# Kernel optimization log

Measured on AMD Instinct MI355X. Metric: run time of the kernel, lower is better.

## Reference

```python
import jax, jax.numpy as jnp
import numpy as np

N_NODES = 50000
N_EDGES = 800000
NEG_SLOPE = 0.2  # PyG GATConv default leaky_relu slope


def gat_conv(x, edge_index, W, a_src, a_dst, b, concat):
    """PyG-style GATConv with self-loops already included in edge_index.
    x: [N, F_in], W: [F_in, H*C], a_src/a_dst: [H, C], b: [H*C] or [C]."""
    N = x.shape[0]
    H, C = a_src.shape
    xw = (x @ W).reshape(N, H, C)                       # [N, H, C]
    src, dst = edge_index[0], edge_index[1]
    alpha_s = jnp.einsum('nhc,hc->nh', xw, a_src)       # [N, H]
    alpha_d = jnp.einsum('nhc,hc->nh', xw, a_dst)
    e = jax.nn.leaky_relu(alpha_s[src] + alpha_d[dst], NEG_SLOPE)  # [E, H]
    # segment softmax over incoming edges of each dst node
    emax = jax.ops.segment_max(e, dst, num_segments=N)  # [N, H]
    p = jnp.exp(e - emax[dst])
    denom = jax.ops.segment_sum(p, dst, num_segments=N)
    alpha = p / (denom[dst] + 1e-16)                    # [E, H]
    msg = xw[src] * alpha[..., None]                    # [E, H, C]
    out = jax.ops.segment_sum(msg, dst, num_segments=N) # [N, H, C]
    out = out.reshape(N, H * C) if concat else out.mean(axis=1)
    return out + b


def setup_inputs() -> dict:
    key = jax.random.key(0)
    ks = jax.random.split(key, 12)
    s = 0.1
    x = jax.random.normal(ks[0], (N_NODES, 128), dtype=jnp.float32)
    edge_index = jax.random.randint(ks[1], (2, N_EDGES), 0, N_NODES, dtype=jnp.int64)
    return {
        'x': x,
        'edge_index': edge_index,
        'W1': jax.random.normal(ks[2], (128, 64), jnp.float32) * s,
        'a1_src': jax.random.normal(ks[3], (8, 8), jnp.float32) * s,
        'a1_dst': jax.random.normal(ks[4], (8, 8), jnp.float32) * s,
        'b1': jnp.zeros((64,), jnp.float32),
        'W2': jax.random.normal(ks[5], (64, 64), jnp.float32) * s,
        'a2_src': jax.random.normal(ks[6], (8, 8), jnp.float32) * s,
        'a2_dst': jax.random.normal(ks[7], (8, 8), jnp.float32) * s,
        'b2': jnp.zeros((64,), jnp.float32),
        'W3': jax.random.normal(ks[8], (64, 242), jnp.float32) * s,
        'a3_src': jax.random.normal(ks[9], (1, 242), jnp.float32) * s,
        'a3_dst': jax.random.normal(ks[10], (1, 242), jnp.float32) * s,
        'b3': jnp.zeros((242,), jnp.float32),
    }


def reference(x, edge_index, W1, a1_src, a1_dst, b1, W2, a2_src, a2_dst, b2,
              W3, a3_src, a3_dst, b3):
    N = x.shape[0]
    # PyG GATConv adds self-loops by default
    loops = jnp.arange(N, dtype=edge_index.dtype)
    ei = jnp.concatenate([edge_index, jnp.stack([loops, loops])], axis=1)
    h = jax.nn.relu(gat_conv(x, ei, W1, a1_src, a1_dst, b1, concat=True))
    # dropout is identity in eval mode
    h = jax.nn.relu(gat_conv(h, ei, W2, a2_src, a2_dst, b2, concat=True))
    h = jax.nn.relu(gat_conv(h, ei, W3, a3_src, a3_dst, b3, concat=False))
    h = h.reshape(N, -1, 2)                             # [N, num_classes, 2]
    return jax.nn.softmax(h, axis=-1)
```

## Files before the change

kernel.cpp:

```cpp
#include <hip/hip_runtime.h>
#include <hip/hip_bf16.h>
#include <hip/hip_fp16.h>


#define CH 4096
#define CAP 8192

__device__ __forceinline__ float lrelu(float s) { return (s >= 0.f) ? s : 0.2f * s; }


__global__ void detect_kernel(const int* __restrict__ ei, int* __restrict__ flag) {
    int t = threadIdx.x;
    int v = ei[2 * t + 1];
    unsigned long long b = __ballot(v == 0);
    if (t == 0) *flag = (b == ~0ULL) ? 1 : 0;
}

__device__ __forceinline__ int edge_at(const void* ei, int is64, long long idx) {
    return is64 ? (int)((const long long*)ei)[idx] : ((const int*)ei)[idx];
}


__global__ void zero_btot_kernel(int* __restrict__ btot) {
    btot[threadIdx.x] = 0;
}

__global__ __launch_bounds__(256)
void histA_kernel(const void* __restrict__ ei, const int* __restrict__ flag,
                  int* __restrict__ blkhist, int* __restrict__ btot, int E, int N) {
    __shared__ int h[256];
    int t = threadIdx.x;
    h[t] = 0;
    __syncthreads();
    int is64 = *flag;
    long long base = (long long)blockIdx.x * CH;
    long long tot = (long long)E + N;
#pragma unroll
    for (int i = 0; i < CH / 256; ++i) {
        long long idx = base + t + i * 256;
        if (idx < tot) {
            int dst = (idx < E) ? edge_at(ei, is64, (long long)E + idx) : (int)(idx - E);
            atomicAdd(&h[(dst >> 8) & 255], 1);
        }
    }
    __syncthreads();
    int nb = (N + 255) >> 8;
    if (t < nb) {
        blkhist[t * 256 + blockIdx.x] = h[t];
        atomicAdd(&btot[t], h[t]);
    }
}

__global__ __launch_bounds__(256)
void bucket_scan_kernel(const int* __restrict__ btot, int* __restrict__ bbase,
                        int nb, int total) {
    __shared__ int s[256];
    int t = threadIdx.x;
    int v = (t < nb) ? btot[t] : 0;
    s[t] = v;
    __syncthreads();
#pragma unroll
    for (int off = 1; off < 256; off <<= 1) {
        int u = (t >= off) ? s[t - off] : 0;
        __syncthreads();
        s[t] += u;
        __syncthreads();
    }
    if (t < nb) bbase[t] = s[t] - v;
    if (t == 0) bbase[nb] = total;
}

__global__ __launch_bounds__(256)
void blk_scan_kernel(const int* __restrict__ blkhist, const int* __restrict__ bbase,
                     int* __restrict__ blkoff, int nblk) {
    __shared__ int s[256];
    int t = threadIdx.x;
    int b = blockIdx.x;
    int v = (t < nblk) ? blkhist[b * 256 + t] : 0;
    s[t] = v;
    __syncthreads();
#pragma unroll
    for (int off = 1; off < 256; off <<= 1) {
        int u = (t >= off) ? s[t - off] : 0;
        __syncthreads();
        s[t] += u;
        __syncthreads();
    }
    if (t < nblk) blkoff[b * 256 + t] = bbase[b] + s[t] - v;
}

__global__ __launch_bounds__(256)
void partC_kernel(const void* __restrict__ ei, const int* __restrict__ flag,
                  const int* __restrict__ blkoff, int2* __restrict__ part,
                  int E, int N) {
    __shared__ int h[256];
    __shared__ int lst[256];
    __shared__ int cur[256];
    __shared__ int grb[256];
    __shared__ int ssrc[CH];
    __shared__ int sdst[CH];
    int t = threadIdx.x;
    h[t] = 0;
    __syncthreads();
    int is64 = *flag;
    long long base = (long long)blockIdx.x * CH;
    long long tot = (long long)E + N;
    int msrc[CH / 256], mdst[CH / 256], mb[CH / 256];
#pragma unroll
    for (int i = 0; i < CH / 256; ++i) {
        long long idx = base + t + i * 256;
        if (idx < tot) {
            int s, d;
            if (idx < E) {
                s = edge_at(ei, is64, idx);
                d = edge_at(ei, is64, (long long)E + idx);
            } else {
                s = (int)(idx - E);
                d = s;
            }
            msrc[i] = s;
            mdst[i] = d;
            mb[i] = (d >> 8) & 255;
            atomicAdd(&h[mb[i]], 1);
        } else {
            mb[i] = -1;
        }
    }
    __syncthreads();
    int v = h[t];
    lst[t] = v;
    __syncthreads();
#pragma unroll
    for (int off = 1; off < 256; off <<= 1) {
        int u = (t >= off) ? lst[t - off] : 0;
        __syncthreads();
        lst[t] += u;
        __syncthreads();
    }
    int ex = lst[t] - v;
    lst[t] = ex;
    cur[t] = ex;
    int nb = (N + 255) >> 8;
    grb[t] = (t < nb) ? blkoff[t * 256 + blockIdx.x] : 0;
    __syncthreads();
#pragma unroll
    for (int i = 0; i < CH / 256; ++i) {
        if (mb[i] >= 0) {
            int slot = atomicAdd(&cur[mb[i]], 1);
            ssrc[slot] = msrc[i];
            sdst[slot] = mdst[i];
        }
    }
    __syncthreads();
    int items = (int)((tot - base < CH) ? (tot - base) : CH);
    for (int r = t; r < items; r += 256) {
        int d = sdst[r];
        int b = (d >> 8) & 255;
        part[grb[b] + (r - lst[b])] = make_int2(ssrc[r], d);
    }
}

__global__ __launch_bounds__(256)
void csrD_kernel(const int2* __restrict__ part, const int* __restrict__ bbase,
                 int* __restrict__ row_ptr, int* __restrict__ adj, int N) {
    __shared__ int cnt[256];
    __shared__ int lst[256];
    __shared__ int cur[256];
    __shared__ int ssrc[CAP];
    int t = threadIdx.x;
    int b = blockIdx.x;
    int lo = bbase[b], hi = bbase[b + 1];
    int n0 = b << 8;
    cnt[t] = 0;
    __syncthreads();
    for (int r = lo + t; r < hi; r += 256) atomicAdd(&cnt[part[r].y & 255], 1);
    __syncthreads();
    int v = cnt[t];
    lst[t] = v;
    __syncthreads();
#pragma unroll
    for (int off = 1; off < 256; off <<= 1) {
        int u = (t >= off) ? lst[t - off] : 0;
        __syncthreads();
        lst[t] += u;
        __syncthreads();
    }
    int ex = lst[t] - v;
    lst[t] = ex;
    cur[t] = ex;
    __syncthreads();
    if (n0 + t < N) row_ptr[n0 + t] = lo + ex;
    if (b == gridDim.x - 1 && t == 0) row_ptr[N] = hi;
    int items = hi - lo;
    if (items <= CAP) {
        for (int r = lo + t; r < hi; r += 256) {
            int2 p = part[r];
            int slot = atomicAdd(&cur[p.y & 255], 1);
            ssrc[slot] = p.x;
        }
        __syncthreads();
        for (int r = t; r < items; r += 256) adj[lo + r] = ssrc[r];
    } else {
        for (int r = lo + t; r < hi; r += 256) {
            int2 p = part[r];
            int slot = atomicAdd(&cur[p.y & 255], 1);
            adj[lo + slot] = p.x;
        }
    }
}


__global__ void w3a_kernel(const float* __restrict__ W3,
                           const float* __restrict__ a3s,
                           const float* __restrict__ a3d,
                           float* __restrict__ w_as, float* __restrict__ w_ad) {
    int t = threadIdx.x;
    if (t >= 128) return;
    int k = t & 63;
    const float* a = (t < 64) ? a3s : a3d;
    float s = 0.f;
    for (int c = 0; c < 242; ++c) s = fmaf(W3[k * 242 + c], a[c], s);
    if (t < 64) w_as[k] = s; else w_ad[k] = s;
}

__global__ __launch_bounds__(256)
void w3pad_kernel(const float* __restrict__ W3, float* __restrict__ W3p) {
    int t = blockIdx.x * blockDim.x + threadIdx.x;
    if (t >= 64 * 244) return;
    int k = t / 244, c = t - k * 244;
    W3p[t] = (c < 242) ? W3[k * 242 + c] : 0.f;
}


template <int K>
__global__ __launch_bounds__(256)
void gemm_alpha_v5(const float* __restrict__ X, const float* __restrict__ W,
                   const float* __restrict__ a_src, const float* __restrict__ a_dst,
                   __half* __restrict__ XWh, float* __restrict__ As, float* __restrict__ Ad,
                   int N) {
    constexpr int S = K + 4;
    constexpr int F4R = K / 4;
    __shared__ float xs[32][S];
    int t = threadIdx.x;
    int block0 = blockIdx.x * 32;

    for (int i = t; i < 32 * F4R; i += 256) {
        int row = i / F4R, c4 = i - row * F4R;
        int node = block0 + row;
        float4 v = (node < N) ? *(const float4*)(X + (size_t)node * K + c4 * 4)
                              : make_float4(0.f, 0.f, 0.f, 0.f);
        *(float4*)(&xs[row][c4 * 4]) = v;
    }
    __syncthreads();

    int wave = t >> 6, lane = t & 63;
    int jj = lane >> 4, cc = lane & 15;
    int r0 = wave * 8 + jj * 2;
    int base = block0 + r0;

    float4 o0 = make_float4(0.f, 0.f, 0.f, 0.f);
    float4 o1 = make_float4(0.f, 0.f, 0.f, 0.f);

    const float* wp = W + cc * 4;
#pragma unroll 2
    for (int k = 0; k < K; k += 4) {
        float4 w0 = *(const float4*)(wp + (size_t)(k + 0) * 64);
        float4 w1 = *(const float4*)(wp + (size_t)(k + 1) * 64);
        float4 w2 = *(const float4*)(wp + (size_t)(k + 2) * 64);
        float4 w3 = *(const float4*)(wp + (size_t)(k + 3) * 64);
        float4 m0 = *(const float4*)(&xs[r0][k]);
        float4 m1 = *(const float4*)(&xs[r0 + 1][k]);

        o0.x = fmaf(m0.x, w0.x, o0.x);
        o0.y = fmaf(m0.x, w0.y, o0.y);
        o0.z = fmaf(m0.x, w0.z, o0.z);
        o0.w = fmaf(m0.x, w0.w, o0.w);
        o0.x = fmaf(m0.y, w1.x, o0.x);
        o0.y = fmaf(m0.y, w1.y, o0.y);
        o0.z = fmaf(m0.y, w1.z, o0.z);
        o0.w = fmaf(m0.y, w1.w, o0.w);
        o0.x = fmaf(m0.z, w2.x, o0.x);
        o0.y = fmaf(m0.z, w2.y, o0.y);
        o0.z = fmaf(m0.z, w2.z, o0.z);
        o0.w = fmaf(m0.z, w2.w, o0.w);
        o0.x = fmaf(m0.w, w3.x, o0.x);
        o0.y = fmaf(m0.w, w3.y, o0.y);
        o0.z = fmaf(m0.w, w3.z, o0.z);
        o0.w = fmaf(m0.w, w3.w, o0.w);

        o1.x = fmaf(m1.x, w0.x, o1.x);
        o1.y = fmaf(m1.x, w0.y, o1.y);
        o1.z = fmaf(m1.x, w0.z, o1.z);
        o1.w = fmaf(m1.x, w0.w, o1.w);
        o1.x = fmaf(m1.y, w1.x, o1.x);
        o1.y = fmaf(m1.y, w1.y, o1.y);
        o1.z = fmaf(m1.y, w1.z, o1.z);
        o1.w = fmaf(m1.y, w1.w, o1.w);
        o1.x = fmaf(m1.z, w2.x, o1.x);
        o1.y = fmaf(m1.z, w2.y, o1.y);
        o1.z = fmaf(m1.z, w2.z, o1.z);
        o1.w = fmaf(m1.z, w2.w, o1.w);
        o1.x = fmaf(m1.w, w3.x, o1.x);
        o1.y = fmaf(m1.w, w3.y, o1.y);
        o1.z = fmaf(m1.w, w3.z, o1.z);
        o1.w = fmaf(m1.w, w3.w, o1.w);
    }

    float4 av = *(const float4*)(a_src + cc * 4);
    float4 dv = *(const float4*)(a_dst + cc * 4);

    if (base < N) {
        union { __half2 h[2]; uint2 u; } pk;
        pk.h[0] = __floats2half2_rn(o0.x, o0.y);
        pk.h[1] = __floats2half2_rn(o0.z, o0.w);
        *(uint2*)(XWh + (size_t)base * 64 + cc * 4) = pk.u;
        float s = o0.x * av.x + o0.y * av.y + o0.z * av.z + o0.w * av.w;
        float d = o0.x * dv.x + o0.y * dv.y + o0.z * dv.z + o0.w * dv.w;
        s += __shfl_xor(s, 1);
        d += __shfl_xor(d, 1);
        if ((cc & 1) == 0) {
            As[base * 8 + (cc >> 1)] = s;
            Ad[base * 8 + (cc >> 1)] = d;
        }
    }
    if (base + 1 < N) {
        union { __half2 h[2]; uint2 u; } pk;
        pk.h[0] = __floats2half2_rn(o1.x, o1.y);
        pk.h[1] = __floats2half2_rn(o1.z, o1.w);
        *(uint2*)(XWh + (size_t)(base + 1) * 64 + cc * 4) = pk.u;
        float s = o1.x * av.x + o1.y * av.y + o1.z * av.z + o1.w * av.w;
        float d = o1.x * dv.x + o1.y * dv.y + o1.z * dv.z + o1.w * dv.w;
        s += __shfl_xor(s, 1);
        d += __shfl_xor(d, 1);
        if ((cc & 1) == 0) {
            As[(base + 1) * 8 + (cc >> 1)] = s;
            Ad[(base + 1) * 8 + (cc >> 1)] = d;
        }
    }
}


template <bool WITH_A3, bool HALF_OUT>
__global__ __launch_bounds__(256)
void agg_h8c8_v3(const __half* __restrict__ XW, const float* __restrict__ As,
                 const float* __restrict__ Ad, const int* __restrict__ row_ptr,
                 const int* __restrict__ adj, const float* __restrict__ bias,
                 void* __restrict__ OUTv,
                 const float* __restrict__ w_as, const float* __restrict__ w_ad,
                 float* __restrict__ As3, float* __restrict__ Ad3, int N) {
    int wave = threadIdx.x >> 6, lane = threadIdx.x & 63;
    int node = blockIdx.x * 4 + wave;
    if (node >= N) return;
    int beg = row_ptr[node], end = row_ptr[node + 1];
    int eP = lane >> 3, hP = lane & 7;
    int hA = lane >> 3;
    float adp = Ad[node * 8 + hP];
    float bv = bias[lane];

    float den_part = 0.f;
    float acc0 = 0.f, acc1 = 0.f;
    int idx = beg;
    for (; idx + 8 <= end; idx += 8) {
        int se = adj[idx + eP];
        float ec = As[(size_t)se * 8 + hP];
        float p = __expf(lrelu(ec + adp));
        den_part += p;
        int s0 = adj[idx + 0], s1 = adj[idx + 1], s2 = adj[idx + 2], s3 = adj[idx + 3];
        int s4 = adj[idx + 4], s5 = adj[idx + 5], s6 = adj[idx + 6], s7 = adj[idx + 7];
        float x0 = __half2float(XW[(size_t)s0 * 64 + lane]);
        float x1 = __half2float(XW[(size_t)s1 * 64 + lane]);
        float x2 = __half2float(XW[(size_t)s2 * 64 + lane]);
        float x3 = __half2float(XW[(size_t)s3 * 64 + lane]);
        float x4 = __half2float(XW[(size_t)s4 * 64 + lane]);
        float x5 = __half2float(XW[(size_t)s5 * 64 + lane]);
        float x6 = __half2float(XW[(size_t)s6 * 64 + lane]);
        float x7 = __half2float(XW[(size_t)s7 * 64 + lane]);
        float p0 = __shfl(p, 0 * 8 + hA);
        float p1 = __shfl(p, 1 * 8 + hA);
        float p2 = __shfl(p, 2 * 8 + hA);
        float p3 = __shfl(p, 3 * 8 + hA);
        float p4 = __shfl(p, 4 * 8 + hA);
        float p5 = __shfl(p, 5 * 8 + hA);
        float p6 = __shfl(p, 6 * 8 + hA);
        float p7 = __shfl(p, 7 * 8 + hA);
        acc0 = fmaf(p0, x0, acc0);
        acc1 = fmaf(p1, x1, acc1);
        acc0 = fmaf(p2, x2, acc0);
        acc1 = fmaf(p3, x3, acc1);
        acc0 = fmaf(p4, x4, acc0);
        acc1 = fmaf(p5, x5, acc1);
        acc0 = fmaf(p6, x6, acc0);
        acc1 = fmaf(p7, x7, acc1);
    }
    int rem = end - idx;
    if (rem > 0) {
        int se = adj[idx + (eP < rem ? eP : rem - 1)];
        float ec = As[(size_t)se * 8 + hP];
        float p = (eP < rem) ? __expf(lrelu(ec + adp)) : 0.f;
        den_part += p;
#pragma unroll
        for (int k = 0; k < 8; ++k) {
            if (k < rem) {
                int sk = adj[idx + k];
                float xk = __half2float(XW[(size_t)sk * 64 + lane]);
                float pk = __shfl(p, k * 8 + hA);
                acc0 = fmaf(pk, xk, acc0);
            }
        }
    }
    float acc = acc0 + acc1;
    den_part += __shfl_xor(den_part, 8);
    den_part += __shfl_xor(den_part, 16);
    den_part += __shfl_xor(den_part, 32);
    float den = __shfl(den_part, hA);

    float v = fmaxf(acc / (den + 1e-16f) + bv, 0.f);
    if (HALF_OUT) ((__half*)OUTv)[(size_t)node * 64 + lane] = __float2half_rn(v);
    else          ((float*)OUTv)[(size_t)node * 64 + lane] = v;

    if (WITH_A3) {
        float s3v = v * w_as[lane];
        float d3v = v * w_ad[lane];
#pragma unroll
        for (int m = 1; m <= 32; m <<= 1) {
            s3v += __shfl_xor(s3v, m);
            d3v += __shfl_xor(d3v, m);
        }
        if (lane == 0) {
            As3[node] = s3v;
            Ad3[node] = d3v;
        }
    }
}


__global__ __launch_bounds__(256)
void agg3msg_v3(const __half* __restrict__ H2, const float* __restrict__ As3,
                const float* __restrict__ Ad3, const int* __restrict__ row_ptr,
                const int* __restrict__ adj, float* __restrict__ MSG, int N) {
    int wave = threadIdx.x >> 6, lane = threadIdx.x & 63;
    int node = blockIdx.x * 4 + wave;
    if (node >= N) return;
    int beg = row_ptr[node], end = row_ptr[node + 1];
    float ad = Ad3[node];
    int eP = lane & 7;
    int gbase = lane & 56;

    float den_part = 0.f;
    float acc0 = 0.f, acc1 = 0.f;
    int idx = beg;
    for (; idx + 8 <= end; idx += 8) {
        int se = adj[idx + eP];
        float p = __expf(lrelu(As3[se] + ad));
        den_part += p;
        int s0 = adj[idx + 0], s1 = adj[idx + 1], s2 = adj[idx + 2], s3 = adj[idx + 3];
        int s4 = adj[idx + 4], s5 = adj[idx + 5], s6 = adj[idx + 6], s7 = adj[idx + 7];
        float x0 = __half2float(H2[(size_t)s0 * 64 + lane]);
        float x1 = __half2float(H2[(size_t)s1 * 64 + lane]);
        float x2 = __half2float(H2[(size_t)s2 * 64 + lane]);
        float x3 = __half2float(H2[(size_t)s3 * 64 + lane]);
        float x4 = __half2float(H2[(size_t)s4 * 64 + lane]);
        float x5 = __half2float(H2[(size_t)s5 * 64 + lane]);
        float x6 = __half2float(H2[(size_t)s6 * 64 + lane]);
        float x7 = __half2float(H2[(size_t)s7 * 64 + lane]);
        float p0 = __shfl(p, gbase + 0);
        float p1 = __shfl(p, gbase + 1);
        float p2 = __shfl(p, gbase + 2);
        float p3 = __shfl(p, gbase + 3);
        float p4 = __shfl(p, gbase + 4);
        float p5 = __shfl(p, gbase + 5);
        float p6 = __shfl(p, gbase + 6);
        float p7 = __shfl(p, gbase + 7);
        acc0 = fmaf(p0, x0, acc0);
        acc1 = fmaf(p1, x1, acc1);
        acc0 = fmaf(p2, x2, acc0);
        acc1 = fmaf(p3, x3, acc1);
        acc0 = fmaf(p4, x4, acc0);
        acc1 = fmaf(p5, x5, acc1);
        acc0 = fmaf(p6, x6, acc0);
        acc1 = fmaf(p7, x7, acc1);
    }
    int rem = end - idx;
    if (rem > 0) {
        int se = adj[idx + (eP < rem ? eP : rem - 1)];
        float p = (eP < rem) ? __expf(lrelu(As3[se] + ad)) : 0.f;
        den_part += p;
#pragma unroll
        for (int k = 0; k < 8; ++k) {
            if (k < rem) {
                int sk = adj[idx + k];
                float xk = __half2float(H2[(size_t)sk * 64 + lane]);
                float pk = __shfl(p, gbase + k);
                acc0 = fmaf(pk, xk, acc0);
            }
        }
    }
    float acc = acc0 + acc1;
    den_part += __shfl_xor(den_part, 1);
    den_part += __shfl_xor(den_part, 2);
    den_part += __shfl_xor(den_part, 4);
    MSG[(size_t)node * 64 + lane] = acc / (den_part + 1e-16f);
}


__global__ __launch_bounds__(256)
void gemm3_kernel(const float* __restrict__ MSG, const float* __restrict__ W3p,
                  const float* __restrict__ bias, float* __restrict__ OUT, int N) {
    __shared__ float msh[4][8][64];
    int wave = threadIdx.x >> 6, lane = threadIdx.x & 63;
    int base = blockIdx.x * 32 + wave * 8;

#pragma unroll
    for (int j = 0; j < 8; ++j) {
        int node = base + j;
        msh[wave][j][lane] = (node < N) ? MSG[(size_t)node * 64 + lane] : 0.f;
    }

    int c0 = lane * 4;
    if (c0 < 242) {
        float o[8][4];
#pragma unroll
        for (int j = 0; j < 8; ++j)
#pragma unroll
            for (int q = 0; q < 4; ++q) o[j][q] = 0.f;

#pragma unroll 4
        for (int k = 0; k < 64; k += 4) {
            float4 w0 = *(const float4*)(W3p + (size_t)(k + 0) * 244 + c0);
            float4 w1 = *(const float4*)(W3p + (size_t)(k + 1) * 244 + c0);
            float4 w2 = *(const float4*)(W3p + (size_t)(k + 2) * 244 + c0);
            float4 w3 = *(const float4*)(W3p + (size_t)(k + 3) * 244 + c0);
#pragma unroll
            for (int j = 0; j < 8; ++j) {
                float4 m = *(const float4*)(&msh[wave][j][k]);
                o[j][0] = fmaf(m.x, w0.x, o[j][0]);
                o[j][1] = fmaf(m.x, w0.y, o[j][1]);
                o[j][2] = fmaf(m.x, w0.z, o[j][2]);
                o[j][3] = fmaf(m.x, w0.w, o[j][3]);
                o[j][0] = fmaf(m.y, w1.x, o[j][0]);
                o[j][1] = fmaf(m.y, w1.y, o[j][1]);
                o[j][2] = fmaf(m.y, w1.z, o[j][2]);
                o[j][3] = fmaf(m.y, w1.w, o[j][3]);
                o[j][0] = fmaf(m.z, w2.x, o[j][0]);
                o[j][1] = fmaf(m.z, w2.y, o[j][1]);
                o[j][2] = fmaf(m.z, w2.z, o[j][2]);
                o[j][3] = fmaf(m.z, w2.w, o[j][3]);
                o[j][0] = fmaf(m.w, w3.x, o[j][0]);
                o[j][1] = fmaf(m.w, w3.y, o[j][1]);
                o[j][2] = fmaf(m.w, w3.z, o[j][2]);
                o[j][3] = fmaf(m.w, w3.w, o[j][3]);
            }
        }

        float b0 = bias[c0], b1v = bias[c0 + 1];
        float b2v = (c0 + 2 < 242) ? bias[c0 + 2] : 0.f;
        float b3v = (c0 + 3 < 242) ? bias[c0 + 3] : 0.f;
#pragma unroll
        for (int j = 0; j < 8; ++j) {
            int node = base + j;
            if (node >= N) break;
            size_t out_base = (size_t)node * 242 + c0;
            float v0 = fmaxf(o[j][0] + b0, 0.f);
            float v1 = fmaxf(o[j][1] + b1v, 0.f);
            float m01 = fmaxf(v0, v1);
            float e0 = __expf(v0 - m01), e1 = __expf(v1 - m01);
            float r01 = 1.f / (e0 + e1);
            OUT[out_base]     = e0 * r01;
            OUT[out_base + 1] = e1 * r01;
            if (c0 + 2 < 242) {
                float v2 = fmaxf(o[j][2] + b2v, 0.f);
                float v3 = fmaxf(o[j][3] + b3v, 0.f);
                float m23 = fmaxf(v2, v3);
                float e2 = __expf(v2 - m23), e3 = __expf(v3 - m23);
                float r23 = 1.f / (e2 + e3);
                OUT[out_base + 2] = e2 * r23;
                OUT[out_base + 3] = e3 * r23;
            }
        }
    }
}


extern "C" void kernel_launch(void* const* d_in, const int* in_sizes, int n_in,
                              void* d_out, int out_size, void* d_ws, size_t ws_size,
                              hipStream_t stream) {
    const float* x   = (const float*)d_in[0];
    const void*  ei  = d_in[1];
    const float* W1  = (const float*)d_in[2];
    const float* a1s = (const float*)d_in[3];
    const float* a1d = (const float*)d_in[4];
    const float* b1  = (const float*)d_in[5];
    const float* W2  = (const float*)d_in[6];
    const float* a2s = (const float*)d_in[7];
    const float* a2d = (const float*)d_in[8];
    const float* b2  = (const float*)d_in[9];
    const float* W3  = (const float*)d_in[10];
    const float* a3s = (const float*)d_in[11];
    const float* a3d = (const float*)d_in[12];
    const float* b3  = (const float*)d_in[13];
    float* out = (float*)d_out;

    const int N = in_sizes[0] / 128;
    const int E = in_sizes[1] / 2;

    char* w = (char*)d_ws;
    auto alloc = [&](size_t bytes) {
        char* p = w;
        w += (bytes + 255) & ~(size_t)255;
        return p;
    };
    int*   flag    = (int*)alloc(4);
    int*   row_ptr = (int*)alloc(((size_t)N + 1) * 4);
    int*   adj     = (int*)alloc((size_t)(E + N) * 4);
    int*   btot    = (int*)alloc(256 * 4);
    int*   bbase   = (int*)alloc(257 * 4);
    float* As      = (float*)alloc((size_t)N * 8 * 4);
    float* Ad      = (float*)alloc((size_t)N * 8 * 4);
    float* As3     = (float*)alloc((size_t)N * 4);
    float* Ad3     = (float*)alloc((size_t)N * 4);
    float* w_as    = (float*)alloc(64 * 4);
    float* w_ad    = (float*)alloc(64 * 4);
    float* W3p     = (float*)alloc((size_t)64 * 244 * 4);
    float* bufA    = (float*)alloc((size_t)N * 64 * 4);
    float* bufB    = (float*)alloc((size_t)N * 64 * 4);
    int2*   part    = (int2*)bufA;
    int*    blkhist = (int*)((char*)bufA + (size_t)7 * 1024 * 1024);
    int*    blkoff  = (int*)((char*)bufA + (size_t)7 * 1024 * 1024 + 256 * 1024);
    __half* XW1h = (__half*)bufA;
    __half* XW2h = (__half*)((char*)bufA + (size_t)N * 64 * 2);
    __half* h2h  = (__half*)bufA;
    float*  msg  = bufB;

    int tot  = E + N;
    int nblk = (tot + CH - 1) / CH;
    int nb   = (N + 255) >> 8;

    detect_kernel<<<1, 64, 0, stream>>>((const int*)ei, flag);
    zero_btot_kernel<<<1, 256, 0, stream>>>(btot);
    histA_kernel<<<nblk, 256, 0, stream>>>(ei, flag, blkhist, btot, E, N);
    bucket_scan_kernel<<<1, 256, 0, stream>>>(btot, bbase, nb, tot);
    blk_scan_kernel<<<nb, 256, 0, stream>>>(blkhist, bbase, blkoff, nblk);
    partC_kernel<<<nblk, 256, 0, stream>>>(ei, flag, blkoff, part, E, N);
    csrD_kernel<<<nb, 256, 0, stream>>>(part, bbase, row_ptr, adj, N);
    w3a_kernel<<<1, 128, 0, stream>>>(W3, a3s, a3d, w_as, w_ad);
    w3pad_kernel<<<(64 * 244 + 255) / 256, 256, 0, stream>>>(W3, W3p);

    int nb4 = (N + 3) / 4;
    int nb32 = (N + 31) / 32;

    gemm_alpha_v5<128><<<nb32, 256, 0, stream>>>(x, W1, a1s, a1d, XW1h, As, Ad, N);
    agg_h8c8_v3<false, false><<<nb4, 256, 0, stream>>>(XW1h, As, Ad, row_ptr, adj, b1,
                                                       bufB, nullptr, nullptr,
                                                       nullptr, nullptr, N);
    gemm_alpha_v5<64><<<nb32, 256, 0, stream>>>(bufB, W2, a2s, a2d, XW2h, As, Ad, N);
    agg_h8c8_v3<true, true><<<nb4, 256, 0, stream>>>(XW2h, As, Ad, row_ptr, adj, b2,
                                                     h2h, w_as, w_ad, As3, Ad3, N);
    agg3msg_v3<<<nb4, 256, 0, stream>>>(h2h, As3, Ad3, row_ptr, adj, msg, N);
    gemm3_kernel<<<nb32, 256, 0, stream>>>(msg, W3p, b3, out, N);
}
```

Before: 365.9 us.

## Split each wave into two half-waves gathering two neighbor rows as half2

The three aggregation kernels now have each 32-lane half-wave gather a different neighbor row with half2 (4-byte) loads, so one wave processes two edges per load step and 16 edges per loop iteration. The two half-wave partial sums are combined with a cross-half shuffle at the end, and only the lower half writes the output. The aim is to cut the number of load instructions per edge and expose more memory-level parallelism in the gather. In exchange it adds select logic in the tail loop, extra register use for the 16 indices, and leaves half the lanes idle during the output writes.

```diff
diff --git a/kernel.cpp b/kernel.cpp
--- a/kernel.cpp
+++ b/kernel.cpp
@@ -342,7 +342,7 @@
 
 template <bool WITH_A3, bool HALF_OUT>
 __global__ __launch_bounds__(256)
-void agg_h8c8_v3(const __half* __restrict__ XW, const float* __restrict__ As,
+void agg_h8c8_v4(const __half2* __restrict__ XW, const float* __restrict__ As,
                  const float* __restrict__ Ad, const int* __restrict__ row_ptr,
                  const int* __restrict__ adj, const float* __restrict__ bias,
                  void* __restrict__ OUTv,
@@ -353,76 +353,75 @@
     if (node >= N) return;
     int beg = row_ptr[node], end = row_ptr[node + 1];
     int eP = lane >> 3, hP = lane & 7;
-    int hA = lane >> 3;
+    int r = lane >> 5, c2 = lane & 31;
+    int hA = c2 >> 2;
     float adp = Ad[node * 8 + hP];
-    float bv = bias[lane];
 
     float den_part = 0.f;
-    float acc0 = 0.f, acc1 = 0.f;
+    float accx = 0.f, accy = 0.f;
     int idx = beg;
-    for (; idx + 8 <= end; idx += 8) {
-        int se = adj[idx + eP];
-        float ec = As[(size_t)se * 8 + hP];
-        float p = __expf(lrelu(ec + adp));
-        den_part += p;
-        int s0 = adj[idx + 0], s1 = adj[idx + 1], s2 = adj[idx + 2], s3 = adj[idx + 3];
-        int s4 = adj[idx + 4], s5 = adj[idx + 5], s6 = adj[idx + 6], s7 = adj[idx + 7];
-        float x0 = __half2float(XW[(size_t)s0 * 64 + lane]);
-        float x1 = __half2float(XW[(size_t)s1 * 64 + lane]);
-        float x2 = __half2float(XW[(size_t)s2 * 64 + lane]);
-        float x3 = __half2float(XW[(size_t)s3 * 64 + lane]);
-        float x4 = __half2float(XW[(size_t)s4 * 64 + lane]);
-        float x5 = __half2float(XW[(size_t)s5 * 64 + lane]);
-        float x6 = __half2float(XW[(size_t)s6 * 64 + lane]);
-        float x7 = __half2float(XW[(size_t)s7 * 64 + lane]);
-        float p0 = __shfl(p, 0 * 8 + hA);
-        float p1 = __shfl(p, 1 * 8 + hA);
-        float p2 = __shfl(p, 2 * 8 + hA);
-        float p3 = __shfl(p, 3 * 8 + hA);
-        float p4 = __shfl(p, 4 * 8 + hA);
-        float p5 = __shfl(p, 5 * 8 + hA);
-        float p6 = __shfl(p, 6 * 8 + hA);
-        float p7 = __shfl(p, 7 * 8 + hA);
-        acc0 = fmaf(p0, x0, acc0);
-        acc1 = fmaf(p1, x1, acc1);
-        acc0 = fmaf(p2, x2, acc0);
-        acc1 = fmaf(p3, x3, acc1);
-        acc0 = fmaf(p4, x4, acc0);
-        acc1 = fmaf(p5, x5, acc1);
-        acc0 = fmaf(p6, x6, acc0);
-        acc1 = fmaf(p7, x7, acc1);
+    for (; idx + 16 <= end; idx += 16) {
+        int sa = adj[idx + eP];
+        int sb = adj[idx + 8 + eP];
+        float pa = __expf(lrelu(As[(size_t)sa * 8 + hP] + adp));
+        float pb = __expf(lrelu(As[(size_t)sb * 8 + hP] + adp));
+        den_part += pa + pb;
+        int s[16];
+#pragma unroll
+        for (int k = 0; k < 16; ++k) s[k] = adj[idx + k];
+#pragma unroll
+        for (int k = 0; k < 16; k += 2) {
+            int row = r ? s[k + 1] : s[k];
+            float2 xv = __half22float2(XW[(size_t)row * 32 + c2]);
+            float psrc = (k < 8) ? pa : pb;
+            float pk = __shfl(psrc, ((k & 7) + r) * 8 + hA);
+            accx = fmaf(pk, xv.x, accx);
+            accy = fmaf(pk, xv.y, accy);
+        }
     }
     int rem = end - idx;
     if (rem > 0) {
-        int se = adj[idx + (eP < rem ? eP : rem - 1)];
-        float ec = As[(size_t)se * 8 + hP];
-        float p = (eP < rem) ? __expf(lrelu(ec + adp)) : 0.f;
-        den_part += p;
-#pragma unroll
-        for (int k = 0; k < 8; ++k) {
-            if (k < rem) {
-                int sk = adj[idx + k];
-                float xk = __half2float(XW[(size_t)sk * 64 + lane]);
-                float pk = __shfl(p, k * 8 + hA);
-                acc0 = fmaf(pk, xk, acc0);
-            }
-        }
-    }
-    float acc = acc0 + acc1;
+        int ca = (eP < rem) ? eP : rem - 1;
+        int cb = (8 + eP < rem) ? 8 + eP : rem - 1;
+        int sa = adj[idx + ca];
+        int sb = adj[idx + cb];
+        float pa = (eP < rem) ? __expf(lrelu(As[(size_t)sa * 8 + hP] + adp)) : 0.f;
+        float pb = (8 + eP < rem) ? __expf(lrelu(As[(size_t)sb * 8 + hP] + adp)) : 0.f;
+        den_part += pa + pb;
+        int s[16];
+#pragma unroll
+        for (int k = 0; k < 16; ++k) s[k] = adj[idx + ((k < rem) ? k : rem - 1)];
+#pragma unroll
+        for (int k = 0; k < 16; k += 2) {
+            if (k >= rem) break;
+            int row = r ? s[(k + 1 < rem) ? k + 1 : rem - 1] : s[k];
+            float2 xv = __half22float2(XW[(size_t)row * 32 + c2]);
+            float psrc = (k < 8) ? pa : pb;
+            float pk = __shfl(psrc, ((k & 7) + r) * 8 + hA);
+            accx = fmaf(pk, xv.x, accx);
+            accy = fmaf(pk, xv.y, accy);
+        }
+    }
+    accx += __shfl_xor(accx, 32);
+    accy += __shfl_xor(accy, 32);
     den_part += __shfl_xor(den_part, 8);
     den_part += __shfl_xor(den_part, 16);
     den_part += __shfl_xor(den_part, 32);
     float den = __shfl(den_part, hA);
 
-    float v = fmaxf(acc / (den + 1e-16f) + bv, 0.f);
-    if (HALF_OUT) ((__half*)OUTv)[(size_t)node * 64 + lane] = __float2half_rn(v);
-    else          ((float*)OUTv)[(size_t)node * 64 + lane] = v;
+    float rden = 1.f / (den + 1e-16f);
+    float vx = fmaxf(accx * rden + bias[c2 * 2], 0.f);
+    float vy = fmaxf(accy * rden + bias[c2 * 2 + 1], 0.f);
+    if (r == 0) {
+        if (HALF_OUT) ((__half2*)OUTv)[(size_t)node * 32 + c2] = __floats2half2_rn(vx, vy);
+        else          ((float2*)OUTv)[(size_t)node * 32 + c2] = make_float2(vx, vy);
+    }
 
     if (WITH_A3) {
-        float s3v = v * w_as[lane];
-        float d3v = v * w_ad[lane];
-#pragma unroll
-        for (int m = 1; m <= 32; m <<= 1) {
+        float s3v = vx * w_as[c2 * 2] + vy * w_as[c2 * 2 + 1];
+        float d3v = vx * w_ad[c2 * 2] + vy * w_ad[c2 * 2 + 1];
+#pragma unroll
+        for (int m = 1; m <= 16; m <<= 1) {
             s3v += __shfl_xor(s3v, m);
             d3v += __shfl_xor(d3v, m);
         }
@@ -435,7 +434,7 @@
 
 
 __global__ __launch_bounds__(256)
-void agg3msg_v3(const __half* __restrict__ H2, const float* __restrict__ As3,
+void agg3msg_v4(const __half2* __restrict__ H2, const float* __restrict__ As3,
                 const float* __restrict__ Ad3, const int* __restrict__ row_ptr,
                 const int* __restrict__ adj, float* __restrict__ MSG, int N) {
     int wave = threadIdx.x >> 6, lane = threadIdx.x & 63;
@@ -443,63 +442,57 @@
     if (node >= N) return;
     int beg = row_ptr[node], end = row_ptr[node + 1];
     float ad = Ad3[node];
-    int eP = lane & 7;
-    int gbase = lane & 56;
+    int eP = lane & 15;
+    int r = lane >> 5, c2 = lane & 31;
 
     float den_part = 0.f;
-    float acc0 = 0.f, acc1 = 0.f;
+    float accx = 0.f, accy = 0.f;
     int idx = beg;
-    for (; idx + 8 <= end; idx += 8) {
+    for (; idx + 16 <= end; idx += 16) {
         int se = adj[idx + eP];
         float p = __expf(lrelu(As3[se] + ad));
         den_part += p;
-        int s0 = adj[idx + 0], s1 = adj[idx + 1], s2 = adj[idx + 2], s3 = adj[idx + 3];
-        int s4 = adj[idx + 4], s5 = adj[idx + 5], s6 = adj[idx + 6], s7 = adj[idx + 7];
-        float x0 = __half2float(H2[(size_t)s0 * 64 + lane]);
-        float x1 = __half2float(H2[(size_t)s1 * 64 + lane]);
-        float x2 = __half2float(H2[(size_t)s2 * 64 + lane]);
-        float x3 = __half2float(H2[(size_t)s3 * 64 + lane]);
-        float x4 = __half2float(H2[(size_t)s4 * 64 + lane]);
-        float x5 = __half2float(H2[(size_t)s5 * 64 + lane]);
-        float x6 = __half2float(H2[(size_t)s6 * 64 + lane]);
-        float x7 = __half2float(H2[(size_t)s7 * 64 + lane]);
-        float p0 = __shfl(p, gbase + 0);
-        float p1 = __shfl(p, gbase + 1);
-        float p2 = __shfl(p, gbase + 2);
-        float p3 = __shfl(p, gbase + 3);
-        float p4 = __shfl(p, gbase + 4);
-        float p5 = __shfl(p, gbase + 5);
-        float p6 = __shfl(p, gbase + 6);
-        float p7 = __shfl(p, gbase + 7);
-        acc0 = fmaf(p0, x0, acc0);
-        acc1 = fmaf(p1, x1, acc1);
-        acc0 = fmaf(p2, x2, acc0);
-        acc1 = fmaf(p3, x3, acc1);
-        acc0 = fmaf(p4, x4, acc0);
-        acc1 = fmaf(p5, x5, acc1);
-        acc0 = fmaf(p6, x6, acc0);
-        acc1 = fmaf(p7, x7, acc1);
+        int s[16];
+#pragma unroll
+        for (int k = 0; k < 16; ++k) s[k] = adj[idx + k];
+#pragma unroll
+        for (int k = 0; k < 16; k += 2) {
+            int row = r ? s[k + 1] : s[k];
+            float2 xv = __half22float2(H2[(size_t)row * 32 + c2]);
+            float pk = __shfl(p, k + r);
+            accx = fmaf(pk, xv.x, accx);
+            accy = fmaf(pk, xv.y, accy);
+        }
     }
     int rem = end - idx;
     if (rem > 0) {
-        int se = adj[idx + (eP < rem ? eP : rem - 1)];
+        int ce = (eP < rem) ? eP : rem - 1;
+        int se = adj[idx + ce];
         float p = (eP < rem) ? __expf(lrelu(As3[se] + ad)) : 0.f;
         den_part += p;
-#pragma unroll
-        for (int k = 0; k < 8; ++k) {
-            if (k < rem) {
-                int sk = adj[idx + k];
-                float xk = __half2float(H2[(size_t)sk * 64 + lane]);
-                float pk = __shfl(p, gbase + k);
-                acc0 = fmaf(pk, xk, acc0);
-            }
-        }
-    }
-    float acc = acc0 + acc1;
+        int s[16];
+#pragma unroll
+        for (int k = 0; k < 16; ++k) s[k] = adj[idx + ((k < rem) ? k : rem - 1)];
+#pragma unroll
+        for (int k = 0; k < 16; k += 2) {
+            if (k >= rem) break;
+            int row = r ? s[(k + 1 < rem) ? k + 1 : rem - 1] : s[k];
+            float2 xv = __half22float2(H2[(size_t)row * 32 + c2]);
+            float pk = __shfl(p, k + r);
+            accx = fmaf(pk, xv.x, accx);
+            accy = fmaf(pk, xv.y, accy);
+        }
+    }
+    accx += __shfl_xor(accx, 32);
+    accy += __shfl_xor(accy, 32);
     den_part += __shfl_xor(den_part, 1);
     den_part += __shfl_xor(den_part, 2);
     den_part += __shfl_xor(den_part, 4);
-    MSG[(size_t)node * 64 + lane] = acc / (den_part + 1e-16f);
+    den_part += __shfl_xor(den_part, 8);
+    float rden = 1.f / (den_part + 1e-16f);
+    if (r == 0) {
+        ((float2*)MSG)[(size_t)node * 32 + c2] = make_float2(accx * rden, accy * rden);
+    }
 }
 
 
@@ -649,12 +642,15 @@
     int nb32 = (N + 31) / 32;
 
     gemm_alpha_v5<128><<<nb32, 256, 0, stream>>>(x, W1, a1s, a1d, XW1h, As, Ad, N);
-    agg_h8c8_v3<false, false><<<nb4, 256, 0, stream>>>(XW1h, As, Ad, row_ptr, adj, b1,
-                                                       bufB, nullptr, nullptr,
+    agg_h8c8_v4<false, false><<<nb4, 256, 0, stream>>>((const __half2*)XW1h, As, Ad,
+                                                       row_ptr, adj, b1, bufB,
+                                                       nullptr, nullptr,
                                                        nullptr, nullptr, N);
     gemm_alpha_v5<64><<<nb32, 256, 0, stream>>>(bufB, W2, a2s, a2d, XW2h, As, Ad, N);
-    agg_h8c8_v3<true, true><<<nb4, 256, 0, stream>>>(XW2h, As, Ad, row_ptr, adj, b2,
-                                                     h2h, w_as, w_ad, As3, Ad3, N);
-    agg3msg_v3<<<nb4, 256, 0, stream>>>(h2h, As3, Ad3, row_ptr, adj, msg, N);
+    agg_h8c8_v4<true, true><<<nb4, 256, 0, stream>>>((const __half2*)XW2h, As, Ad,
+                                                     row_ptr, adj, b2, h2h,
+                                                     w_as, w_ad, As3, Ad3, N);
+    agg3msg_v4<<<nb4, 256, 0, stream>>>((const __half2*)h2h, As3, Ad3, row_ptr, adj,
+                                        msg, N);
     gemm3_kernel<<<nb32, 256, 0, stream>>>(msg, W3p, b3, out, N);
 }
```

Result: slower. 439.3 us (+20.1%).
